# Kernel tuning notes

Hardware: AMD Instinct MI355X
Metric: run time of the kernel (lower is better)

Reference implementation:

```python
import jax, jax.numpy as jnp
import numpy as np

B_, S_, D_, N_, R_ = 2, 2048, 1024, 16, 64  # batch, seq, d_model, d_state, dt_rank


def setup_inputs() -> dict:
    key = jax.random.key(0)
    ks = jax.random.split(key, 12)
    x = jax.random.normal(ks[0], (B_, S_, D_), dtype=jnp.float32)
    # params (xavier-ish scale)
    W_dtw = jax.random.normal(ks[1], (R_, D_), dtype=jnp.float32) * (1.0 / np.sqrt(D_))
    W_dt = jax.random.normal(ks[2], (D_, R_), dtype=jnp.float32) * (1.0 / np.sqrt(R_))
    b_dt = jnp.zeros((D_,), dtype=jnp.float32)
    A_log = jnp.log(jax.random.uniform(ks[3], (D_, N_), minval=0.5, maxval=1.5, dtype=jnp.float32))
    W_B = jax.random.normal(ks[4], (N_, D_), dtype=jnp.float32) * (1.0 / np.sqrt(D_))
    W_C = jax.random.normal(ks[5], (N_, D_), dtype=jnp.float32) * (1.0 / np.sqrt(D_))
    Dp = jnp.ones((D_,), dtype=jnp.float32)
    ln_g = jnp.ones((D_,), dtype=jnp.float32)
    ln_b = jnp.zeros((D_,), dtype=jnp.float32)
    W_out = jax.random.normal(ks[6], (D_, D_), dtype=jnp.float32) * (1.0 / np.sqrt(D_))
    return {"x": x, "W_dtw": W_dtw, "W_dt": W_dt, "b_dt": b_dt, "A_log": A_log,
            "W_B": W_B, "W_C": W_C, "Dp": Dp, "ln_g": ln_g, "ln_b": ln_b, "W_out": W_out}


def _layernorm(y, g, b, eps=1e-5):
    mu = jnp.mean(y, axis=-1, keepdims=True)
    var = jnp.mean(jnp.square(y - mu), axis=-1, keepdims=True)
    return (y - mu) * jax.lax.rsqrt(var + eps) * g + b


def reference(x, W_dtw, W_dt, b_dt, A_log, W_B, W_C, Dp, ln_g, ln_b, W_out):
    # projections
    dt = jnp.einsum('bsd,rd->bsr', x, W_dtw)                 # [B,S,R]
    delta = jax.nn.softplus(jnp.einsum('bsr,dr->bsd', dt, W_dt) + b_dt)  # [B,S,D]
    Bm = jnp.einsum('bsd,nd->bsn', x, W_B)                   # [B,S,N]
    Cm = jnp.einsum('bsd,nd->bsn', x, W_C)                   # [B,S,N]
    A = -jnp.exp(A_log)                                      # [D,N]

    def step(h, inp):
        d_t, b_t, c_t, x_t = inp                             # [B,D],[B,N],[B,N],[B,D]
        dA = jnp.exp(d_t[..., None] * A)                     # [B,D,N]
        h = dA * h + (d_t[..., None] * b_t[:, None, :]) * x_t[..., None]
        y_t = jnp.sum(h * c_t[:, None, :], axis=-1)          # [B,D]
        return h, y_t

    h0 = jnp.zeros((x.shape[0], x.shape[2], A.shape[1]), dtype=x.dtype)
    xs = (jnp.swapaxes(delta, 0, 1), jnp.swapaxes(Bm, 0, 1),
          jnp.swapaxes(Cm, 0, 1), jnp.swapaxes(x, 0, 1))
    _, ys = jax.lax.scan(step, h0, xs)                       # ys: [S,B,D]
    y = jnp.swapaxes(ys, 0, 1) + Dp * x                      # [B,S,D]
    y = _layernorm(y, ln_g, ln_b)
    return jnp.einsum('bsd,ed->bse', y, W_out)
```

## Files before the change

### kernel.cpp

```cpp
#include <hip/hip_runtime.h>
#include <hip/hip_bf16.h>

#define B_ 2
#define S_ 2048
#define D_ 1024
#define N_ 16
#define R_ 64
#define NC 64
#define CL 32
#define BS_ (B_*S_)

typedef __attribute__((ext_vector_type(4))) float f32x4;
typedef __attribute__((ext_vector_type(8))) short bf16x8;
typedef __attribute__((ext_vector_type(8))) unsigned short u16x8;

__device__ __forceinline__ unsigned short f2b(float v) {
  unsigned u = __builtin_bit_cast(unsigned, v);
  unsigned r = ((u >> 16) & 1u) + 0x7FFFu;
  return (unsigned short)((u + r) >> 16);
}

__device__ __forceinline__ void gload_lds16(const void* g, void* l) {
  __builtin_amdgcn_global_load_lds(
      (const __attribute__((address_space(1))) unsigned int*)g,
      (__attribute__((address_space(3))) unsigned int*)l, 16, 0, 0);
}

__global__ __launch_bounds__(256) void k_cast(const float* __restrict__ s,
                                              unsigned short* __restrict__ d, int n) {
  int i = (blockIdx.x * 256 + threadIdx.x) * 4;
  if (i >= n) return;
  float4 v = *(const float4*)&s[i];
  ushort4 o;
  o.x = f2b(v.x); o.y = f2b(v.y); o.z = f2b(v.z); o.w = f2b(v.w);
  *(ushort4*)&d[i] = o;
}

__global__ __launch_bounds__(256) void k_proj(
    const unsigned short* __restrict__ xb, const unsigned short* __restrict__ Wcat,
    float* __restrict__ part) {
  __shared__ __align__(16) unsigned short Xs[2][64 * 64];
  __shared__ __align__(16) unsigned short Ws[2][96 * 64];
  const int tid = threadIdx.x;
  const int lane = tid & 63, w = tid >> 6;
  const size_t row0 = (size_t)blockIdx.x * 64;
  const int kbase = blockIdx.y * 256;
  f32x4 acc[6] = {};

  auto stage = [&](int buf, int k0) {
    #pragma unroll
    for (int i = 0; i < 2; ++i) {
      int id = i * 256 + tid; int row = id >> 3, s = id & 7;
      gload_lds16(xb + (row0 + row) * D_ + k0 + ((s ^ (row & 7)) << 3),
                  Xs[buf] + row * 64 + s * 8);
    }
    #pragma unroll
    for (int i = 0; i < 3; ++i) {
      int id = i * 256 + tid; int row = id >> 3, s = id & 7;
      gload_lds16(Wcat + (size_t)row * D_ + k0 + ((s ^ (row & 7)) << 3),
                  Ws[buf] + row * 64 + s * 8);
    }
  };
  stage(0, kbase);
  __syncthreads();
  int cur = 0;
  const int r = lane & 15, kg = lane >> 4;
  for (int t = 0; t < 4; ++t) {
    if (t < 3) stage(cur ^ 1, kbase + (t + 1) * 64);
    #pragma unroll
    for (int ks = 0; ks < 2; ++ks) {
      const int arow = w * 16 + r;
      bf16x8 a = *(const bf16x8*)&Xs[cur][arow * 64 + ((((ks << 2) | kg) ^ (arow & 7)) << 3)];
      #pragma unroll
      for (int nt = 0; nt < 6; ++nt) {
        const int brow = nt * 16 + r;
        bf16x8 b = *(const bf16x8*)&Ws[cur][brow * 64 + ((((ks << 2) | kg) ^ (brow & 7)) << 3)];
        acc[nt] = __builtin_amdgcn_mfma_f32_16x16x32_bf16(a, b, acc[nt], 0, 0, 0);
      }
    }
    __syncthreads();
    cur ^= 1;
  }
  const int cr = lane >> 4, cc = lane & 15;
  float* pb = part + (size_t)blockIdx.y * (BS_ * 96);
  #pragma unroll
  for (int nt = 0; nt < 6; ++nt)
    #pragma unroll
    for (int j = 0; j < 4; ++j)
      pb[(row0 + w * 16 + cr * 4 + j) * 96 + nt * 16 + cc] = acc[nt][j];
}

__global__ __launch_bounds__(256) void k_projred(
    const float* __restrict__ part, unsigned short* __restrict__ dtb,
    float* __restrict__ Bm, float* __restrict__ Cm) {
  int e = blockIdx.x * 256 + threadIdx.x;
  int row = e / 96, col = e - row * 96;
  float s = part[e] + part[e + BS_ * 96] + part[e + 2 * BS_ * 96] + part[e + 3 * BS_ * 96];
  if (col < 64)      dtb[row * R_ + col] = f2b(s);
  else if (col < 80) Bm[row * N_ + col - 64] = s;
  else               Cm[row * N_ + col - 80] = s;
}

__global__ __launch_bounds__(256) void k_delta(
    const unsigned short* __restrict__ dtb, const unsigned short* __restrict__ wdtb,
    const float* __restrict__ b_dt, float* __restrict__ delta) {
  __shared__ __align__(16) unsigned short As[128 * 64];
  __shared__ __align__(16) unsigned short Bs[128 * 64];
  const int tid = threadIdx.x;
  const int lane = tid & 63, wid = tid >> 6;
  const int wr = wid >> 1, wc = wid & 1;
  const size_t row0 = (size_t)blockIdx.x * 128;
  const size_t col0 = (size_t)blockIdx.y * 128;
  f32x4 acc[4][4] = {};

  {
    const int r = tid >> 3, s = tid & 7;
    #pragma unroll
    for (int i = 0; i < 4; ++i) {
      const int row = i * 32 + r;
      const int gs = s ^ (row & 7);
      gload_lds16(dtb + (row0 + row) * R_ + gs * 8, As + row * 64 + s * 8);
      gload_lds16(wdtb + (col0 + row) * R_ + gs * 8, Bs + row * 64 + s * 8);
    }
  }
  __syncthreads();
  const int r = lane & 15, kg = lane >> 4;
  #pragma unroll
  for (int ks = 0; ks < 2; ++ks) {
    bf16x8 a[4], b[4];
    #pragma unroll
    for (int m = 0; m < 4; ++m) {
      const int arow = wr * 64 + m * 16 + r;
      a[m] = *(const bf16x8*)&As[arow * 64 + (((ks << 2) | kg) ^ (arow & 7)) * 8];
    }
    #pragma unroll
    for (int n = 0; n < 4; ++n) {
      const int brow = wc * 64 + n * 16 + r;
      b[n] = *(const bf16x8*)&Bs[brow * 64 + (((ks << 2) | kg) ^ (brow & 7)) * 8];
    }
    #pragma unroll
    for (int m = 0; m < 4; ++m)
      #pragma unroll
      for (int n = 0; n < 4; ++n)
        acc[m][n] = __builtin_amdgcn_mfma_f32_16x16x32_bf16(a[m], b[n], acc[m][n], 0, 0, 0);
  }
  const int cr = lane >> 4, cc = lane & 15;
  #pragma unroll
  for (int m = 0; m < 4; ++m) {
    #pragma unroll
    for (int n = 0; n < 4; ++n) {
      const int d = (int)col0 + wc * 64 + n * 16 + cc;
      const float bd = b_dt[d];
      #pragma unroll
      for (int j = 0; j < 4; ++j) {
        size_t trow = row0 + wr * 64 + m * 16 + cr * 4 + j;
        float v = acc[m][n][j] + bd;
        float sp = fmaxf(v, 0.f) + log1pf(__expf(-fabsf(v)));
        delta[trow * D_ + d] = sp;
      }
    }
  }
}

__global__ __launch_bounds__(256) void k_scan1(
    const float* __restrict__ x, const float* __restrict__ delta,
    const float* __restrict__ Bm, const float* __restrict__ A_log,
    float* __restrict__ aprod, float* __restrict__ hend) {
  int g = blockIdx.x * 256 + threadIdx.x;
  int nq = g & 3;
  int d = (g >> 2) & (D_ - 1);
  int c = (g >> 12) & (NC - 1);
  int b = g >> 18;

  float4 av = *(const float4*)&A_log[(size_t)d * N_ + nq * 4];
  float Ad[4] = {-__expf(av.x), -__expf(av.y), -__expf(av.z), -__expf(av.w)};
  float ap[4] = {1.f, 1.f, 1.f, 1.f}, h[4] = {0.f, 0.f, 0.f, 0.f};

  size_t base = (size_t)(b * S_ + c * CL) * D_ + d;
  size_t bcb  = (size_t)(b * S_ + c * CL) * N_ + nq * 4;
  for (int s = 0; s < CL; ++s) {
    float dlt = delta[base + (size_t)s * D_];
    float xv  = x[base + (size_t)s * D_];
    float dbx = dlt * xv;
    float4 Bv = *(const float4*)&Bm[bcb + (size_t)s * N_];
    float da0 = __expf(dlt * Ad[0]), da1 = __expf(dlt * Ad[1]);
    float da2 = __expf(dlt * Ad[2]), da3 = __expf(dlt * Ad[3]);
    ap[0] *= da0; ap[1] *= da1; ap[2] *= da2; ap[3] *= da3;
    h[0] = da0 * h[0] + dbx * Bv.x;
    h[1] = da1 * h[1] + dbx * Bv.y;
    h[2] = da2 * h[2] + dbx * Bv.z;
    h[3] = da3 * h[3] + dbx * Bv.w;
  }
  size_t o = (((size_t)(b * NC + c)) * D_ + d) * N_ + nq * 4;
  *(float4*)&aprod[o] = make_float4(ap[0], ap[1], ap[2], ap[3]);
  *(float4*)&hend[o]  = make_float4(h[0], h[1], h[2], h[3]);
}

__global__ __launch_bounds__(256) void k_scan2(
    const float* __restrict__ aprod, const float* __restrict__ hend,
    float* __restrict__ hstart) {
  int g = blockIdx.x * 256 + threadIdx.x;
  int n = g & (N_ - 1);
  int d = (g >> 4) & (D_ - 1);
  int b = g >> 14;
  float h = 0.f;
  for (int c = 0; c < NC; ++c) {
    size_t idx = (((size_t)b * NC + c) * D_ + d) * N_ + n;
    hstart[idx] = h;
    h = aprod[idx] * h + hend[idx];
  }
}

__global__ __launch_bounds__(256) void k_scan3(
    const float* __restrict__ x, const float* __restrict__ delta,
    const float* __restrict__ Bm, const float* __restrict__ Cm,
    const float* __restrict__ A_log, const float* __restrict__ hstart,
    const float* __restrict__ Dp, float* __restrict__ ypre) {
  int g = blockIdx.x * 256 + threadIdx.x;
  int nq = g & 3;
  int d = (g >> 2) & (D_ - 1);
  int c = (g >> 12) & (NC - 1);
  int b = g >> 18;

  float4 av = *(const float4*)&A_log[(size_t)d * N_ + nq * 4];
  float Ad[4] = {-__expf(av.x), -__expf(av.y), -__expf(av.z), -__expf(av.w)};
  float h[4];
  {
    size_t o = (((size_t)(b * NC + c)) * D_ + d) * N_ + nq * 4;
    float4 v = *(const float4*)&hstart[o];
    h[0] = v.x; h[1] = v.y; h[2] = v.z; h[3] = v.w;
  }
  const float Dpd = Dp[d];

  size_t base = (size_t)(b * S_ + c * CL) * D_ + d;
  size_t bcb  = (size_t)(b * S_ + c * CL) * N_ + nq * 4;
  for (int s = 0; s < CL; ++s) {
    float dlt = delta[base + (size_t)s * D_];
    float xv  = x[base + (size_t)s * D_];
    float dbx = dlt * xv;
    float4 Bv = *(const float4*)&Bm[bcb + (size_t)s * N_];
    float4 Cv = *(const float4*)&Cm[bcb + (size_t)s * N_];
    float da0 = __expf(dlt * Ad[0]), da1 = __expf(dlt * Ad[1]);
    float da2 = __expf(dlt * Ad[2]), da3 = __expf(dlt * Ad[3]);
    h[0] = da0 * h[0] + dbx * Bv.x;
    h[1] = da1 * h[1] + dbx * Bv.y;
    h[2] = da2 * h[2] + dbx * Bv.z;
    h[3] = da3 * h[3] + dbx * Bv.w;
    float y = h[0] * Cv.x + h[1] * Cv.y + h[2] * Cv.z + h[3] * Cv.w;
    y += __shfl_xor(y, 1);
    y += __shfl_xor(y, 2);
    if (nq == 0) ypre[base + (size_t)s * D_] = y + Dpd * xv;
  }
}

__device__ __forceinline__ float block_sum256(float v, float* sm) {
  #pragma unroll
  for (int o = 32; o > 0; o >>= 1) v += __shfl_down(v, o, 64);
  int w = threadIdx.x >> 6;
  __syncthreads();
  if ((threadIdx.x & 63) == 0) sm[w] = v;
  __syncthreads();
  return (sm[0] + sm[1]) + (sm[2] + sm[3]);
}

__global__ __launch_bounds__(256) void k_ln(
    const float* __restrict__ ypre, const float* __restrict__ g,
    const float* __restrict__ bta, unsigned short* __restrict__ ybf) {
  __shared__ float sm[4];
  const int t = blockIdx.x;
  const int tid = threadIdx.x;
  size_t base = (size_t)t * D_ + tid * 4;
  float4 v = *(const float4*)&ypre[base];
  float s1 = block_sum256(v.x + v.y + v.z + v.w, sm);
  float mu = s1 * (1.f / D_);
  float cx = v.x - mu, cy = v.y - mu, cz = v.z - mu, cw = v.w - mu;
  float s2 = block_sum256(cx*cx + cy*cy + cz*cz + cw*cw, sm);
  float rs = rsqrtf(s2 * (1.f / D_) + 1e-5f);
  float4 gg = *(const float4*)&g[tid * 4];
  float4 bb = *(const float4*)&bta[tid * 4];
  ushort4 o;
  o.x = f2b(cx * rs * gg.x + bb.x);
  o.y = f2b(cy * rs * gg.y + bb.y);
  o.z = f2b(cz * rs * gg.z + bb.z);
  o.w = f2b(cw * rs * gg.w + bb.w);
  *(ushort4*)&ybf[base] = o;
}

__device__ __forceinline__ void stage128x64(const unsigned short* __restrict__ g,
                                            size_t row0, int k0,
                                            unsigned short* lds, int tid) {
  const int r = tid >> 3, s = tid & 7;
  #pragma unroll
  for (int i = 0; i < 4; ++i) {
    const int row = i * 32 + r;
    const int gs = s ^ (row & 7);
    gload_lds16(g + ((row0 + row) << 10) + k0 + (gs << 3), lds + row * 64 + s * 8);
  }
}

__global__ __launch_bounds__(256) void k_out(const unsigned short* __restrict__ Y,
                                             const unsigned short* __restrict__ W,
                                             float* __restrict__ O) {
  __shared__ __align__(16) unsigned short As[2][128 * 64];
  __shared__ __align__(16) unsigned short Bs[2][128 * 64];
  const int tid = threadIdx.x;
  const int lane = tid & 63, wid = tid >> 6;
  const int wr = wid >> 1, wc = wid & 1;
  const size_t row0 = (size_t)blockIdx.x * 128;
  const size_t col0 = (size_t)blockIdx.y * 128;
  f32x4 acc[4][4] = {};

  stage128x64(Y, row0, 0, As[0], tid);
  stage128x64(W, col0, 0, Bs[0], tid);
  __syncthreads();

  int cur = 0;
  const int r = lane & 15, kg = lane >> 4;
  for (int t = 0; t < 16; ++t) {
    if (t + 1 < 16) {
      stage128x64(Y, row0, (t + 1) * 64, As[cur ^ 1], tid);
      stage128x64(W, col0, (t + 1) * 64, Bs[cur ^ 1], tid);
    }
    #pragma unroll
    for (int ks = 0; ks < 2; ++ks) {
      bf16x8 a[4], b[4];
      #pragma unroll
      for (int m = 0; m < 4; ++m) {
        const int arow = wr * 64 + m * 16 + r;
        a[m] = *(const bf16x8*)&As[cur][arow * 64 + (((ks << 2) | kg) ^ (arow & 7)) * 8];
      }
      #pragma unroll
      for (int n = 0; n < 4; ++n) {
        const int brow = wc * 64 + n * 16 + r;
        b[n] = *(const bf16x8*)&Bs[cur][brow * 64 + (((ks << 2) | kg) ^ (brow & 7)) * 8];
      }
      #pragma unroll
      for (int m = 0; m < 4; ++m)
        #pragma unroll
        for (int n = 0; n < 4; ++n)
          acc[m][n] = __builtin_amdgcn_mfma_f32_16x16x32_bf16(a[m], b[n], acc[m][n], 0, 0, 0);
    }
    __syncthreads();
    cur ^= 1;
  }

  const int cr = lane >> 4, cc = lane & 15;
  #pragma unroll
  for (int m = 0; m < 4; ++m) {
    #pragma unroll
    for (int n = 0; n < 4; ++n) {
      size_t orow = row0 + wr * 64 + m * 16 + cr * 4;
      float* op = O + orow * D_ + col0 + wc * 64 + n * 16 + cc;
      #pragma unroll
      for (int j = 0; j < 4; ++j) op[(size_t)j * D_] = acc[m][n][j];
    }
  }
}

extern "C" void kernel_launch(void* const* d_in, const int* in_sizes, int n_in,
                              void* d_out, int out_size, void* d_ws, size_t ws_size,
                              hipStream_t stream) {
  const float* x     = (const float*)d_in[0];
  const float* W_dtw = (const float*)d_in[1];
  const float* W_dt  = (const float*)d_in[2];
  const float* b_dt  = (const float*)d_in[3];
  const float* A_log = (const float*)d_in[4];
  const float* W_B   = (const float*)d_in[5];
  const float* W_C   = (const float*)d_in[6];
  const float* Dp    = (const float*)d_in[7];
  const float* ln_g  = (const float*)d_in[8];
  const float* ln_b  = (const float*)d_in[9];
  const float* W_out = (const float*)d_in[10];
  float* out = (float*)d_out;

  float* ws = (float*)d_ws;
  float* delta  = ws;
  float* ypre   = delta + (size_t)BS_ * D_;
  float* Bm     = ypre + (size_t)BS_ * D_;
  float* Cm     = Bm + (size_t)BS_ * N_;
  float* aprod  = Cm + (size_t)BS_ * N_;
  float* hend   = aprod + (size_t)B_ * NC * D_ * N_;
  float* hstart = hend + (size_t)B_ * NC * D_ * N_;
  unsigned short* xb   = (unsigned short*)aprod;
  float*          part = hend;
  unsigned short* dtb  = (unsigned short*)hstart;
  unsigned short* wdtb = dtb + (size_t)BS_ * R_;
  unsigned short* Wcat = wdtb + (size_t)D_ * R_;
  unsigned short* ybf  = (unsigned short*)aprod;
  unsigned short* wob  = (unsigned short*)hend;

  k_cast<<<dim3(4096), dim3(256), 0, stream>>>(x, xb, BS_ * D_);
  k_cast<<<dim3(64),   dim3(256), 0, stream>>>(W_dtw, Wcat, R_ * D_);
  k_cast<<<dim3(16),   dim3(256), 0, stream>>>(W_B, Wcat + (size_t)R_ * D_, N_ * D_);
  k_cast<<<dim3(16),   dim3(256), 0, stream>>>(W_C, Wcat + (size_t)(R_ + N_) * D_, N_ * D_);
  k_cast<<<dim3(64),   dim3(256), 0, stream>>>(W_dt, wdtb, D_ * R_);

  k_proj<<<dim3(BS_ / 64, 4), dim3(256), 0, stream>>>(xb, Wcat, part);
  k_projred<<<dim3(BS_ * 96 / 256), dim3(256), 0, stream>>>(part, dtb, Bm, Cm);
  k_delta<<<dim3(BS_ / 128, D_ / 128), dim3(256), 0, stream>>>(dtb, wdtb, b_dt, delta);

  k_scan1<<<dim3(B_ * NC * D_ * 4 / 256), dim3(256), 0, stream>>>(x, delta, Bm, A_log,
                                                                  aprod, hend);
  k_scan2<<<dim3(B_ * D_ * N_ / 256), dim3(256), 0, stream>>>(aprod, hend, hstart);
  k_cast<<<dim3(1024), dim3(256), 0, stream>>>(W_out, wob, D_ * D_);
  k_scan3<<<dim3(B_ * NC * D_ * 4 / 256), dim3(256), 0, stream>>>(x, delta, Bm, Cm,
                                                                  A_log, hstart, Dp, ypre);
  k_ln<<<dim3(BS_), dim3(256), 0, stream>>>(ypre, ln_g, ln_b, ybf);
  k_out<<<dim3(BS_ / 128, D_ / 128), dim3(256), 0, stream>>>(ybf, wob, out);
}
```

Before: 129.6 us.

## Fuse all casts into one launch, raise proj K-split, shrink out-GEMM tile

Merges the six separate fp32-to-bf16 cast launches, including the W_out cast, into a single kernel that picks source and destination by index range. This removes launch overhead. The projection GEMM's K-split goes from 4 to 8 so more blocks are in flight, at the cost of more partial sums for the reduction kernel to read. The output GEMM tile is narrowed from 128x128 to 128x64, doubling the grid to fill more CUs. The workspace is relaid out with dedicated regions, so buffers no longer alias.

```diff
diff --git a/kernel.cpp b/kernel.cpp
--- a/kernel.cpp
+++ b/kernel.cpp
@@ -9,6 +9,7 @@
 #define NC 64
 #define CL 32
 #define BS_ (B_*S_)
+#define KSPLIT 8
 
 typedef __attribute__((ext_vector_type(4))) float f32x4;
 typedef __attribute__((ext_vector_type(8))) short bf16x8;
@@ -26,17 +27,28 @@
       (__attribute__((address_space(3))) unsigned int*)l, 16, 0, 0);
 }
 
-__global__ __launch_bounds__(256) void k_cast(const float* __restrict__ s,
-                                              unsigned short* __restrict__ d, int n) {
+__global__ __launch_bounds__(256) void k_castall(
+    const float* __restrict__ x, const float* __restrict__ W_dtw,
+    const float* __restrict__ W_B, const float* __restrict__ W_C,
+    const float* __restrict__ W_dt, const float* __restrict__ W_out,
+    unsigned short* __restrict__ xb, unsigned short* __restrict__ Wcat,
+    unsigned short* __restrict__ wdtb, unsigned short* __restrict__ wob) {
   int i = (blockIdx.x * 256 + threadIdx.x) * 4;
-  if (i >= n) return;
-  float4 v = *(const float4*)&s[i];
+  const float* s; unsigned short* d; int off;
+  if (i < 4194304)      { s = x;     d = xb;           off = 0; }
+  else if (i < 4259840) { s = W_dtw; d = Wcat;         off = 4194304; }
+  else if (i < 4276224) { s = W_B;   d = Wcat + 65536; off = 4259840; }
+  else if (i < 4292608) { s = W_C;   d = Wcat + 81920; off = 4276224; }
+  else if (i < 4358144) { s = W_dt;  d = wdtb;         off = 4292608; }
+  else                  { s = W_out; d = wob;          off = 4358144; }
+  int j = i - off;
+  float4 v = *(const float4*)&s[j];
   ushort4 o;
   o.x = f2b(v.x); o.y = f2b(v.y); o.z = f2b(v.z); o.w = f2b(v.w);
-  *(ushort4*)&d[i] = o;
-}
-
-__global__ __launch_bounds__(256) void k_proj(
+  *(ushort4*)&d[j] = o;
+}
+
+__global__ __launch_bounds__(256, 2) void k_proj(
     const unsigned short* __restrict__ xb, const unsigned short* __restrict__ Wcat,
     float* __restrict__ part) {
   __shared__ __align__(16) unsigned short Xs[2][64 * 64];
@@ -44,7 +56,7 @@
   const int tid = threadIdx.x;
   const int lane = tid & 63, w = tid >> 6;
   const size_t row0 = (size_t)blockIdx.x * 64;
-  const int kbase = blockIdx.y * 256;
+  const int kbase = blockIdx.y * (D_ / KSPLIT);
   f32x4 acc[6] = {};
 
   auto stage = [&](int buf, int k0) {
@@ -65,8 +77,8 @@
   __syncthreads();
   int cur = 0;
   const int r = lane & 15, kg = lane >> 4;
-  for (int t = 0; t < 4; ++t) {
-    if (t < 3) stage(cur ^ 1, kbase + (t + 1) * 64);
+  for (int t = 0; t < 2; ++t) {
+    if (t < 1) stage(cur ^ 1, kbase + 64);
     #pragma unroll
     for (int ks = 0; ks < 2; ++ks) {
       const int arow = w * 16 + r;
@@ -95,7 +107,9 @@
     float* __restrict__ Bm, float* __restrict__ Cm) {
   int e = blockIdx.x * 256 + threadIdx.x;
   int row = e / 96, col = e - row * 96;
-  float s = part[e] + part[e + BS_ * 96] + part[e + 2 * BS_ * 96] + part[e + 3 * BS_ * 96];
+  float s = 0.f;
+  #pragma unroll
+  for (int p = 0; p < KSPLIT; ++p) s += part[e + (size_t)p * (BS_ * 96)];
   if (col < 64)      dtb[row * R_ + col] = f2b(s);
   else if (col < 80) Bm[row * N_ + col - 64] = s;
   else               Cm[row * N_ + col - 80] = s;
@@ -298,20 +312,31 @@
   }
 }
 
-__global__ __launch_bounds__(256) void k_out(const unsigned short* __restrict__ Y,
-                                             const unsigned short* __restrict__ W,
-                                             float* __restrict__ O) {
+__device__ __forceinline__ void stage64x64(const unsigned short* __restrict__ g,
+                                           size_t row0, int k0,
+                                           unsigned short* lds, int tid) {
+  const int r = tid >> 3, s = tid & 7;
+  #pragma unroll
+  for (int i = 0; i < 2; ++i) {
+    const int row = i * 32 + r;
+    const int gs = s ^ (row & 7);
+    gload_lds16(g + ((row0 + row) << 10) + k0 + (gs << 3), lds + row * 64 + s * 8);
+  }
+}
+
+__global__ __launch_bounds__(256, 2) void k_out(const unsigned short* __restrict__ Y,
+                                                const unsigned short* __restrict__ W,
+                                                float* __restrict__ O) {
   __shared__ __align__(16) unsigned short As[2][128 * 64];
-  __shared__ __align__(16) unsigned short Bs[2][128 * 64];
+  __shared__ __align__(16) unsigned short Bs[2][64 * 64];
   const int tid = threadIdx.x;
   const int lane = tid & 63, wid = tid >> 6;
-  const int wr = wid >> 1, wc = wid & 1;
   const size_t row0 = (size_t)blockIdx.x * 128;
-  const size_t col0 = (size_t)blockIdx.y * 128;
-  f32x4 acc[4][4] = {};
+  const size_t col0 = (size_t)blockIdx.y * 64;
+  f32x4 acc[2][4] = {};
 
   stage128x64(Y, row0, 0, As[0], tid);
-  stage128x64(W, col0, 0, Bs[0], tid);
+  stage64x64(W, col0, 0, Bs[0], tid);
   __syncthreads();
 
   int cur = 0;
@@ -319,23 +344,23 @@
   for (int t = 0; t < 16; ++t) {
     if (t + 1 < 16) {
       stage128x64(Y, row0, (t + 1) * 64, As[cur ^ 1], tid);
-      stage128x64(W, col0, (t + 1) * 64, Bs[cur ^ 1], tid);
+      stage64x64(W, col0, (t + 1) * 64, Bs[cur ^ 1], tid);
     }
     #pragma unroll
     for (int ks = 0; ks < 2; ++ks) {
-      bf16x8 a[4], b[4];
-      #pragma unroll
-      for (int m = 0; m < 4; ++m) {
-        const int arow = wr * 64 + m * 16 + r;
+      bf16x8 a[2], b[4];
+      #pragma unroll
+      for (int m = 0; m < 2; ++m) {
+        const int arow = wid * 32 + m * 16 + r;
         a[m] = *(const bf16x8*)&As[cur][arow * 64 + (((ks << 2) | kg) ^ (arow & 7)) * 8];
       }
       #pragma unroll
       for (int n = 0; n < 4; ++n) {
-        const int brow = wc * 64 + n * 16 + r;
+        const int brow = n * 16 + r;
         b[n] = *(const bf16x8*)&Bs[cur][brow * 64 + (((ks << 2) | kg) ^ (brow & 7)) * 8];
       }
       #pragma unroll
-      for (int m = 0; m < 4; ++m)
+      for (int m = 0; m < 2; ++m)
         #pragma unroll
         for (int n = 0; n < 4; ++n)
           acc[m][n] = __builtin_amdgcn_mfma_f32_16x16x32_bf16(a[m], b[n], acc[m][n], 0, 0, 0);
@@ -346,11 +371,11 @@
 
   const int cr = lane >> 4, cc = lane & 15;
   #pragma unroll
-  for (int m = 0; m < 4; ++m) {
+  for (int m = 0; m < 2; ++m) {
     #pragma unroll
     for (int n = 0; n < 4; ++n) {
-      size_t orow = row0 + wr * 64 + m * 16 + cr * 4;
-      float* op = O + orow * D_ + col0 + wc * 64 + n * 16 + cc;
+      size_t orow = row0 + wid * 32 + m * 16 + cr * 4;
+      float* op = O + orow * D_ + col0 + n * 16 + cc;
       #pragma unroll
       for (int j = 0; j < 4; ++j) op[(size_t)j * D_] = acc[m][n][j];
     }
@@ -375,36 +400,30 @@
 
   float* ws = (float*)d_ws;
   float* delta  = ws;
-  float* ypre   = delta + (size_t)BS_ * D_;
-  float* Bm     = ypre + (size_t)BS_ * D_;
-  float* Cm     = Bm + (size_t)BS_ * N_;
-  float* aprod  = Cm + (size_t)BS_ * N_;
-  float* hend   = aprod + (size_t)B_ * NC * D_ * N_;
-  float* hstart = hend + (size_t)B_ * NC * D_ * N_;
-  unsigned short* xb   = (unsigned short*)aprod;
-  float*          part = hend;
-  unsigned short* dtb  = (unsigned short*)hstart;
-  unsigned short* wdtb = dtb + (size_t)BS_ * R_;
-  unsigned short* Wcat = wdtb + (size_t)D_ * R_;
-  unsigned short* ybf  = (unsigned short*)aprod;
-  unsigned short* wob  = (unsigned short*)hend;
-
-  k_cast<<<dim3(4096), dim3(256), 0, stream>>>(x, xb, BS_ * D_);
-  k_cast<<<dim3(64),   dim3(256), 0, stream>>>(W_dtw, Wcat, R_ * D_);
-  k_cast<<<dim3(16),   dim3(256), 0, stream>>>(W_B, Wcat + (size_t)R_ * D_, N_ * D_);
-  k_cast<<<dim3(16),   dim3(256), 0, stream>>>(W_C, Wcat + (size_t)(R_ + N_) * D_, N_ * D_);
-  k_cast<<<dim3(64),   dim3(256), 0, stream>>>(W_dt, wdtb, D_ * R_);
-
-  k_proj<<<dim3(BS_ / 64, 4), dim3(256), 0, stream>>>(xb, Wcat, part);
+  float* ypre   = delta  + (size_t)BS_ * D_;
+  float* Bm     = ypre   + (size_t)BS_ * D_;
+  float* Cm     = Bm     + (size_t)BS_ * N_;
+  float* aprod  = Cm     + (size_t)BS_ * N_;
+  float* hend   = aprod  + (size_t)B_ * NC * D_ * N_;
+  float* hstart = hend   + (size_t)B_ * NC * D_ * N_;
+  float* part   = hstart + (size_t)B_ * NC * D_ * N_;
+  unsigned short* xb   = (unsigned short*)(part + (size_t)KSPLIT * BS_ * 96);
+  unsigned short* Wcat = xb   + (size_t)BS_ * D_;
+  unsigned short* wdtb = Wcat + (size_t)96 * D_;
+  unsigned short* wob  = wdtb + (size_t)D_ * R_;
+  unsigned short* ybf  = wob  + (size_t)D_ * D_;
+  unsigned short* dtb  = ybf  + (size_t)BS_ * D_;
+
+  k_castall<<<dim3(5280), dim3(256), 0, stream>>>(x, W_dtw, W_B, W_C, W_dt, W_out,
+                                                  xb, Wcat, wdtb, wob);
+  k_proj<<<dim3(BS_ / 64, KSPLIT), dim3(256), 0, stream>>>(xb, Wcat, part);
   k_projred<<<dim3(BS_ * 96 / 256), dim3(256), 0, stream>>>(part, dtb, Bm, Cm);
   k_delta<<<dim3(BS_ / 128, D_ / 128), dim3(256), 0, stream>>>(dtb, wdtb, b_dt, delta);
-
   k_scan1<<<dim3(B_ * NC * D_ * 4 / 256), dim3(256), 0, stream>>>(x, delta, Bm, A_log,
                                                                   aprod, hend);
   k_scan2<<<dim3(B_ * D_ * N_ / 256), dim3(256), 0, stream>>>(aprod, hend, hstart);
-  k_cast<<<dim3(1024), dim3(256), 0, stream>>>(W_out, wob, D_ * D_);
   k_scan3<<<dim3(B_ * NC * D_ * 4 / 256), dim3(256), 0, stream>>>(x, delta, Bm, Cm,
                                                                   A_log, hstart, Dp, ypre);
   k_ln<<<dim3(BS_), dim3(256), 0, stream>>>(ypre, ln_g, ln_b, ybf);
-  k_out<<<dim3(BS_ / 128, D_ / 128), dim3(256), 0, stream>>>(ybf, wob, out);
-}
+  k_out<<<dim3(BS_ / 128, D_ / 64), dim3(256), 0, stream>>>(ybf, wob, out);
+}
```

Result: faster. 114.9 us (-11.3%).
